# Kernel tuning notes

Measured on AMD Instinct MI355X. Metric: run time of the kernel, lower is better.

Reference implementation:

```python
import jax, jax.numpy as jnp
import numpy as np

NS = 150            # number of MC weight samples
D_IN, D_H, D_OUT = 1024, 512, 256


def setup_inputs() -> dict:
    key = jax.random.key(0)
    ks = jax.random.split(key, 9)
    x = jax.random.normal(ks[0], (32, D_IN), dtype=jnp.float32)
    # variational means (mu network params)
    mu_W1 = jax.random.normal(ks[1], (D_H, D_IN), dtype=jnp.float32) * 0.02
    mu_b1 = jnp.zeros((D_H,), dtype=jnp.float32)
    mu_W2 = jax.random.normal(ks[2], (D_OUT, D_H), dtype=jnp.float32) * 0.02
    mu_b2 = jnp.zeros((D_OUT,), dtype=jnp.float32)
    # variational log-stds (std network params v); std = exp(v)
    v_W1 = -3.0 + 0.1 * jax.random.normal(ks[3], (D_H, D_IN), dtype=jnp.float32)
    v_b1 = -3.0 + 0.1 * jax.random.normal(ks[4], (D_H,), dtype=jnp.float32)
    v_W2 = -3.0 + 0.1 * jax.random.normal(ks[5], (D_OUT, D_H), dtype=jnp.float32)
    v_b2 = -3.0 + 0.1 * jax.random.normal(ks[6], (D_OUT,), dtype=jnp.float32)
    return {
        "x": x,
        "mu_W1": mu_W1, "mu_b1": mu_b1, "mu_W2": mu_W2, "mu_b2": mu_b2,
        "v_W1": v_W1, "v_b1": v_b1, "v_W2": v_W2, "v_b2": v_b2,
    }


def reference(x, mu_W1, mu_b1, mu_W2, mu_b2, v_W1, v_b1, v_W2, v_b2):
    # Reparameterization: w = mu + eps * sqrt(exp(2v)) = mu + eps * exp(v)
    nk = jax.random.split(jax.random.key(42), 4)
    eW1 = jax.random.normal(nk[0], (NS,) + mu_W1.shape, dtype=mu_W1.dtype)
    eb1 = jax.random.normal(nk[1], (NS,) + mu_b1.shape, dtype=mu_b1.dtype)
    eW2 = jax.random.normal(nk[2], (NS,) + mu_W2.shape, dtype=mu_W2.dtype)
    eb2 = jax.random.normal(nk[3], (NS,) + mu_b2.shape, dtype=mu_b2.dtype)

    W1 = mu_W1 + eW1 * jnp.exp(v_W1)          # [ns, H, I]
    b1 = mu_b1 + eb1 * jnp.exp(v_b1)          # [ns, H]
    W2 = mu_W2 + eW2 * jnp.exp(v_W2)          # [ns, O, H]
    b2 = mu_b2 + eb2 * jnp.exp(v_b2)          # [ns, O]

    # MLP forward, batched over the ns sample axis
    h = jax.nn.relu(jnp.einsum('bi,nhi->nbh', x, W1) + b1[:, None, :])  # [ns, B, H]
    y = jnp.einsum('nbh,noh->nbo', h, W2) + b2[:, None, :]              # [ns, B, O]
    return y  # stacked MC outputs, [ns, B, O]
```

## Files before the change

kernel.cpp:

```cpp
#include <hip/hip_runtime.h>
#include <stdint.h>

#define NS 150
#define D_IN 1024
#define D_H 512
#define D_OUT 256

typedef __bf16 bf16x8 __attribute__((ext_vector_type(8)));
typedef float f32x4 __attribute__((ext_vector_type(4)));

#define OFF_XF    0u
#define OFF_MS1T  16384u
#define OFF_MS2T  1064960u
#define OFF_B1S   1327104u
#define OFF_B2S   1403904u
#define OFF_HB    1442304u

#define SQ2 1.41421354f

#define DSQ2 1.4142135623730951
#define DA  (-0.6931471805599453)
#define ZC3 ((float)(DSQ2 * -4.39150654e-06 * DA*DA*DA*DA*DA))
#define ZC4 ((float)(DSQ2 * 0.00021858087   * DA*DA*DA*DA))
#define ZC5 ((float)(DSQ2 * -0.00125372503  * DA*DA*DA))
#define ZC6 ((float)(DSQ2 * -0.00417768164  * DA*DA))
#define ZC7 ((float)(DSQ2 * 0.246640727     * DA))
#define ZC8 ((float)(DSQ2 * 1.50140941))
#define ZSHIFT 3.6067376022224085f
#define ZCUT  -7.213475204444817f

#define TT0 (SQ2 * -0.000200214257f)
#define TT1 (SQ2 * 0.000100950558f)
#define TT2 (SQ2 * 0.00134934322f)
#define TT3 (SQ2 * -0.00367342844f)
#define TT4 (SQ2 * 0.00573950773f)
#define TT5 (SQ2 * -0.0076224613f)
#define TT6 (SQ2 * 0.00943887047f)
#define TT7 (SQ2 * 1.00167406f)
#define TT8 (SQ2 * 2.83297682f)

#define ROTL32(x, r) __builtin_rotateleft32((x), (r))

__host__ __device__ __forceinline__ void threefry2x32(uint32_t k0, uint32_t k1,
                                                      uint32_t x0, uint32_t x1,
                                                      uint32_t& o0, uint32_t& o1) {
  uint32_t k2 = k0 ^ k1 ^ 0x1BD11BDAu;
  x0 += k0; x1 += k1;
#define TFR(r) { x0 += x1; x1 = ROTL32(x1, r); x1 ^= x0; }
  TFR(13) TFR(15) TFR(26) TFR(6)
  x0 += k1; x1 += k2 + 1u;
  TFR(17) TFR(29) TFR(16) TFR(24)
  x0 += k2; x1 += k0 + 2u;
  TFR(13) TFR(15) TFR(26) TFR(6)
  x0 += k0; x1 += k1 + 3u;
  TFR(17) TFR(29) TFR(16) TFR(24)
  x0 += k1; x1 += k2 + 4u;
  TFR(13) TFR(15) TFR(26) TFR(6)
  x0 += k2; x1 += k0 + 5u;
#undef TFR
  o0 = x0; o1 = x1;
}

__device__ __forceinline__ float tf_normal(uint32_t k0, uint32_t k1, uint32_t idx) {
  uint32_t o0, o1;
  threefry2x32(k0, k1, 0u, idx, o0, o1);
  uint32_t bits = o0 ^ o1;
  uint32_t fb = (bits >> 9) | 0x3F800000u;
  float m = __uint_as_float(fb);
  const float lo = -0.99999994f;
  float u = fmaxf(fmaf(m, 2.0f, -3.0f), lo);
  float t = fmaf(u, -u, 1.0f);
  float w = -0.69314718056f * __builtin_amdgcn_logf(t);
  float p;
  if (w < 5.0f) {
    float ww = w - 2.5f;
    p = SQ2 * 2.81022636e-08f;
    p = fmaf(p, ww, SQ2 * 3.43273939e-07f);
    p = fmaf(p, ww, SQ2 * -3.5233877e-06f);
    p = fmaf(p, ww, SQ2 * -4.39150654e-06f);
    p = fmaf(p, ww, SQ2 * 0.00021858087f);
    p = fmaf(p, ww, SQ2 * -0.00125372503f);
    p = fmaf(p, ww, SQ2 * -0.00417768164f);
    p = fmaf(p, ww, SQ2 * 0.246640727f);
    p = fmaf(p, ww, SQ2 * 1.50140941f);
  } else {
    float ww = __builtin_amdgcn_sqrtf(w) - 3.0f;
    p = TT0;
    p = fmaf(p, ww, TT1); p = fmaf(p, ww, TT2); p = fmaf(p, ww, TT3);
    p = fmaf(p, ww, TT4); p = fmaf(p, ww, TT5); p = fmaf(p, ww, TT6);
    p = fmaf(p, ww, TT7); p = fmaf(p, ww, TT8);
  }
  return p * u;
}

#define TF_ADD8 \
  "v_add_u32 %[a0], %[a0], %[b0]\n\t" "v_add_u32 %[a1], %[a1], %[b1]\n\t" \
  "v_add_u32 %[a2], %[a2], %[b2]\n\t" "v_add_u32 %[a3], %[a3], %[b3]\n\t" \
  "v_add_u32 %[a4], %[a4], %[b4]\n\t" "v_add_u32 %[a5], %[a5], %[b5]\n\t" \
  "v_add_u32 %[a6], %[a6], %[b6]\n\t" "v_add_u32 %[a7], %[a7], %[b7]\n\t"
#define TF_ROT8(sh) \
  "v_alignbit_b32 %[b0], %[b0], %[b0], " sh "\n\t" \
  "v_alignbit_b32 %[b1], %[b1], %[b1], " sh "\n\t" \
  "v_alignbit_b32 %[b2], %[b2], %[b2], " sh "\n\t" \
  "v_alignbit_b32 %[b3], %[b3], %[b3], " sh "\n\t" \
  "v_alignbit_b32 %[b4], %[b4], %[b4], " sh "\n\t" \
  "v_alignbit_b32 %[b5], %[b5], %[b5], " sh "\n\t" \
  "v_alignbit_b32 %[b6], %[b6], %[b6], " sh "\n\t" \
  "v_alignbit_b32 %[b7], %[b7], %[b7], " sh "\n\t"
#define TF_XOR8 \
  "v_xor_b32 %[b0], %[b0], %[a0]\n\t" "v_xor_b32 %[b1], %[b1], %[a1]\n\t" \
  "v_xor_b32 %[b2], %[b2], %[a2]\n\t" "v_xor_b32 %[b3], %[b3], %[a3]\n\t" \
  "v_xor_b32 %[b4], %[b4], %[a4]\n\t" "v_xor_b32 %[b5], %[b5], %[a5]\n\t" \
  "v_xor_b32 %[b6], %[b6], %[a6]\n\t" "v_xor_b32 %[b7], %[b7], %[a7]\n\t"
#define TF_ROUND(sh) TF_ADD8 TF_ROT8(sh) TF_XOR8
#define TF_R1(sh) \
  "v_add_u32 %[a0], %[k0], %[b0]\n\t" "v_add_u32 %[a1], %[k0], %[b1]\n\t" \
  "v_add_u32 %[a2], %[k0], %[b2]\n\t" "v_add_u32 %[a3], %[k0], %[b3]\n\t" \
  "v_add_u32 %[a4], %[k0], %[b4]\n\t" "v_add_u32 %[a5], %[k0], %[b5]\n\t" \
  "v_add_u32 %[a6], %[k0], %[b6]\n\t" "v_add_u32 %[a7], %[k0], %[b7]\n\t" \
  TF_ROT8(sh) TF_XOR8
#define TF_BADD8(KB) \
  "v_add_u32 %[b0], " KB ", %[b0]\n\t" "v_add_u32 %[b1], " KB ", %[b1]\n\t" \
  "v_add_u32 %[b2], " KB ", %[b2]\n\t" "v_add_u32 %[b3], " KB ", %[b3]\n\t" \
  "v_add_u32 %[b4], " KB ", %[b4]\n\t" "v_add_u32 %[b5], " KB ", %[b5]\n\t" \
  "v_add_u32 %[b6], " KB ", %[b6]\n\t" "v_add_u32 %[b7], " KB ", %[b7]\n\t"
#define TF_AADD8(KA) \
  "v_add_u32 %[a0], " KA ", %[a0]\n\t" "v_add_u32 %[a1], " KA ", %[a1]\n\t" \
  "v_add_u32 %[a2], " KA ", %[a2]\n\t" "v_add_u32 %[a3], " KA ", %[a3]\n\t" \
  "v_add_u32 %[a4], " KA ", %[a4]\n\t" "v_add_u32 %[a5], " KA ", %[a5]\n\t" \
  "v_add_u32 %[a6], " KA ", %[a6]\n\t" "v_add_u32 %[a7], " KA ", %[a7]\n\t"
#define TF_A3F(KA) \
  "v_add3_u32 %[a0], %[a0], %[b0], " KA "\n\t" \
  "v_add3_u32 %[a1], %[a1], %[b1], " KA "\n\t" \
  "v_add3_u32 %[a2], %[a2], %[b2], " KA "\n\t" \
  "v_add3_u32 %[a3], %[a3], %[b3], " KA "\n\t" \
  "v_add3_u32 %[a4], %[a4], %[b4], " KA "\n\t" \
  "v_add3_u32 %[a5], %[a5], %[b5], " KA "\n\t" \
  "v_add3_u32 %[a6], %[a6], %[b6], " KA "\n\t" \
  "v_add3_u32 %[a7], %[a7], %[b7], " KA "\n\t"
#define TF_RFOLD(KB, KA, sh) TF_BADD8(KB) TF_A3F(KA) TF_ROT8(sh) TF_XOR8

__device__ __forceinline__ void tf8_bits(uint32_t k0, uint32_t k1, uint32_t k2,
                                         uint32_t idx0, uint32_t* bits) {
  uint32_t k2p1 = k2 + 1u, k0p2 = k0 + 2u, k1p3 = k1 + 3u;
  uint32_t k2p4 = k2 + 4u, k0p5 = k0 + 5u;
  uint32_t t0 = idx0 + k1;
  uint32_t a0, a1, a2, a3, a4, a5, a6, a7;
  uint32_t b0 = t0, b1 = t0 + 1u, b2 = t0 + 2u, b3 = t0 + 3u;
  uint32_t b4 = t0 + 4u, b5 = t0 + 5u, b6 = t0 + 6u, b7 = t0 + 7u;
  asm(TF_R1("19") TF_ROUND("17") TF_ROUND("6") TF_ROUND("26")
      TF_RFOLD("%[k2p1]", "%[k1]", "15")
      TF_ROUND("3") TF_ROUND("16") TF_ROUND("8")
      TF_RFOLD("%[k0p2]", "%[k2]", "19")
      TF_ROUND("17") TF_ROUND("6") TF_ROUND("26")
      TF_RFOLD("%[k1p3]", "%[k0]", "15")
      TF_ROUND("3") TF_ROUND("16") TF_ROUND("8")
      TF_RFOLD("%[k2p4]", "%[k1]", "19")
      TF_ROUND("17") TF_ROUND("6") TF_ROUND("26")
      TF_AADD8("%[k2]") TF_BADD8("%[k0p5]")
      : [a0]"=&v"(a0), [a1]"=&v"(a1), [a2]"=&v"(a2), [a3]"=&v"(a3),
        [a4]"=&v"(a4), [a5]"=&v"(a5), [a6]"=&v"(a6), [a7]"=&v"(a7),
        [b0]"+v"(b0), [b1]"+v"(b1), [b2]"+v"(b2), [b3]"+v"(b3),
        [b4]"+v"(b4), [b5]"+v"(b5), [b6]"+v"(b6), [b7]"+v"(b7)
      : [k0]"s"(k0), [k1]"s"(k1), [k2]"s"(k2), [k2p1]"s"(k2p1),
        [k0p2]"s"(k0p2), [k1p3]"s"(k1p3), [k2p4]"s"(k2p4), [k0p5]"s"(k0p5));
  bits[0] = a0 ^ b0; bits[1] = a1 ^ b1; bits[2] = a2 ^ b2; bits[3] = a3 ^ b3;
  bits[4] = a4 ^ b4; bits[5] = a5 ^ b5; bits[6] = a6 ^ b6; bits[7] = a7 ^ b7;
}

__device__ __forceinline__ float bits_normal(uint32_t bits) {
  uint32_t fb = (bits >> 9) | 0x3F800000u;
  float m = __uint_as_float(fb);
  const float lo = -0.99999994f;
  float u = fmaxf(fmaf(m, 2.0f, -3.0f), lo);
  float t = fmaf(u, -u, 1.0f);
  float z = __builtin_amdgcn_logf(t);
  float p;
  if (z > ZCUT) {
    float zz = z + ZSHIFT;
    p = ZC3;
    p = fmaf(p, zz, ZC4); p = fmaf(p, zz, ZC5); p = fmaf(p, zz, ZC6);
    p = fmaf(p, zz, ZC7); p = fmaf(p, zz, ZC8);
  } else {
    float w = -0.69314718056f * z;
    float ww = __builtin_amdgcn_sqrtf(w) - 3.0f;
    p = TT0;
    p = fmaf(p, ww, TT1); p = fmaf(p, ww, TT2); p = fmaf(p, ww, TT3);
    p = fmaf(p, ww, TT4); p = fmaf(p, ww, TT5); p = fmaf(p, ww, TT6);
    p = fmaf(p, ww, TT7); p = fmaf(p, ww, TT8);
  }
  return p * u;
}

__global__ __launch_bounds__(256) void prep_kernel(
    const float* __restrict__ x,
    const float* __restrict__ muW1, const float* __restrict__ vW1,
    const float* __restrict__ muW2, const float* __restrict__ vW2,
    const float* __restrict__ mub1, const float* __restrict__ vb1,
    const float* __restrict__ mub2, const float* __restrict__ vb2,
    float* __restrict__ ws,
    uint32_t kb1_0, uint32_t kb1_1, uint32_t kb2_0, uint32_t kb2_1) {
  int bb = blockIdx.x;
  int tid = threadIdx.x;
  if (bb < 2048) {
    int t = bb * 256 + tid;
    ((float2*)(ws + OFF_MS1T))[t] = make_float2(muW1[t], expf(vW1[t]));
  } else if (bb < 2560) {
    int t = (bb - 2048) * 256 + tid;
    ((float2*)(ws + OFF_MS2T))[t] = make_float2(muW2[t], expf(vW2[t]));
  } else if (bb < 2688) {
    int t = (bb - 2560) * 256 + tid;
    int j = t & 7, lane = (t >> 3) & 63, fidx = t >> 9;
    int s = fidx >> 1, f = fidx & 1;
    int b = f * 16 + (lane & 15);
    int k = s * 32 + ((lane >> 4) << 3) + j;
    ((__bf16*)(ws + OFF_XF))[t] = (__bf16)x[b * D_IN + k];
  } else if (bb < 2988) {
    int t = (bb - 2688) * 256 + tid;
    int h = t & 511;
    float eps = tf_normal(kb1_0, kb1_1, (uint32_t)t);
    ws[OFF_B1S + t] = fmaf(eps, expf(vb1[h]), mub1[h]);
  } else {
    int t = (bb - 2988) * 256 + tid;
    int o = t & 255;
    float eps = tf_normal(kb2_0, kb2_1, (uint32_t)t);
    ws[OFF_B2S + t] = fmaf(eps, expf(vb2[o]), mub2[o]);
  }
}

__global__ __launch_bounds__(256) void l1_kernel(
    const float* __restrict__ ws, uint32_t k0, uint32_t k1) {
  const float2* __restrict__ ms1 = (const float2*)(ws + OFF_MS1T);
  const bf16x8* __restrict__ xf = (const bf16x8*)(ws + OFF_XF);
  const float* __restrict__ b1s = ws + OFF_B1S;
  __bf16* __restrict__ hB = (__bf16*)(ws + OFF_HB);
  uint32_t k2 = k0 ^ k1 ^ 0x1BD11BDAu;

  __shared__ f32x4 lred[2][2][64];

  int lane = threadIdx.x & 63;
  int wib = threadIdx.x >> 6;
  int pairIdx = wib >> 1, khalf = wib & 1;
  int tile = blockIdx.x * 2 + pairIdx;
  int n = tile >> 5;
  int ht = tile & 31;
  int mrow = lane & 15, quad = lane >> 4;
  int h = ht * 16 + mrow;
  uint32_t base = ((uint32_t)(n * 512 + h)) << 10;
  const float2* __restrict__ msrow = ms1 + (size_t)h * D_IN;

  f32x4 acc0 = {0.f, 0.f, 0.f, 0.f}, acc1 = {0.f, 0.f, 0.f, 0.f};

  int send = khalf * 16 + 16;
  for (int s = khalf * 16; s < send; ++s) {
    int kq = s * 32 + quad * 8;
    const f32x4* msq = (const f32x4*)(msrow + kq);
    f32x4 q0 = msq[0], q1 = msq[1], q2 = msq[2], q3 = msq[3];
    bf16x8 b0 = xf[(s * 2 + 0) * 64 + lane];
    bf16x8 b1 = xf[(s * 2 + 1) * 64 + lane];
    uint32_t bits[8];
    tf8_bits(k0, k1, k2, base + (uint32_t)kq, bits);
    float mu[8], sd[8];
    mu[0]=q0[0]; sd[0]=q0[1]; mu[1]=q0[2]; sd[1]=q0[3];
    mu[2]=q1[0]; sd[2]=q1[1]; mu[3]=q1[2]; sd[3]=q1[3];
    mu[4]=q2[0]; sd[4]=q2[1]; mu[5]=q2[2]; sd[5]=q2[3];
    mu[6]=q3[0]; sd[6]=q3[1]; mu[7]=q3[2]; sd[7]=q3[3];
    bf16x8 a;
#pragma unroll
    for (int j = 0; j < 8; ++j) {
      float eps = bits_normal(bits[j]);
      a[j] = (__bf16)fmaf(eps, sd[j], mu[j]);
    }
    acc0 = __builtin_amdgcn_mfma_f32_16x16x32_bf16(a, b0, acc0, 0, 0, 0);
    acc1 = __builtin_amdgcn_mfma_f32_16x16x32_bf16(a, b1, acc1, 0, 0, 0);
  }

  if (khalf) {
    lred[pairIdx][0][lane] = acc0;
    lred[pairIdx][1][lane] = acc1;
  }
  __syncthreads();
  if (!khalf) {
    f32x4 r0 = lred[pairIdx][0][lane], r1 = lred[pairIdx][1][lane];
    acc0 += r0; acc1 += r1;
    int hq = ht * 16 + quad * 4;
    float4 bias = *(const float4*)(b1s + n * 512 + hq);
    float bv[4] = {bias.x, bias.y, bias.z, bias.w};
    union { __bf16 v[4]; uint2 u; } p0, p1;
#pragma unroll
    for (int r = 0; r < 4; ++r) {
      p0.v[r] = (__bf16)fmaxf(acc0[r] + bv[r], 0.0f);
      p1.v[r] = (__bf16)fmaxf(acc1[r] + bv[r], 0.0f);
    }
    *(uint2*)(hB + ((size_t)(n * 32 + mrow) * 512 + hq)) = p0.u;
    *(uint2*)(hB + ((size_t)(n * 32 + 16 + mrow) * 512 + hq)) = p1.u;
  }
}

__global__ __launch_bounds__(256) void l2_kernel(
    const float* __restrict__ ws, float* __restrict__ y,
    uint32_t k0, uint32_t k1) {
  const float2* __restrict__ ms2 = (const float2*)(ws + OFF_MS2T);
  const bf16x8* __restrict__ hB8 = (const bf16x8*)(ws + OFF_HB);
  const float* __restrict__ b2s = ws + OFF_B2S;
  uint32_t k2 = k0 ^ k1 ^ 0x1BD11BDAu;

  __shared__ f32x4 lred[2][2][64];

  int lane = threadIdx.x & 63;
  int wib = threadIdx.x >> 6;
  int pairIdx = wib >> 1, khalf = wib & 1;
  int tile = blockIdx.x * 2 + pairIdx;
  int n = tile >> 4;
  int ot = tile & 15;
  int mrow = lane & 15, quad = lane >> 4;
  int o = ot * 16 + mrow;
  uint32_t base = (uint32_t)(n * 256 + o) << 9;
  const float2* __restrict__ msrow = ms2 + (size_t)o * D_H;

  f32x4 acc0 = {0.f, 0.f, 0.f, 0.f}, acc1 = {0.f, 0.f, 0.f, 0.f};

  int send = khalf * 8 + 8;
  for (int s = khalf * 8; s < send; ++s) {
    int kq = s * 32 + quad * 8;
    const f32x4* msq = (const f32x4*)(msrow + kq);
    f32x4 q0 = msq[0], q1 = msq[1], q2 = msq[2], q3 = msq[3];
    bf16x8 b0 = hB8[(size_t)(n * 32 + mrow) * 64 + s * 4 + quad];
    bf16x8 b1 = hB8[(size_t)(n * 32 + 16 + mrow) * 64 + s * 4 + quad];
    uint32_t bits[8];
    tf8_bits(k0, k1, k2, base + (uint32_t)kq, bits);
    float mu[8], sd[8];
    mu[0]=q0[0]; sd[0]=q0[1]; mu[1]=q0[2]; sd[1]=q0[3];
    mu[2]=q1[0]; sd[2]=q1[1]; mu[3]=q1[2]; sd[3]=q1[3];
    mu[4]=q2[0]; sd[4]=q2[1]; mu[5]=q2[2]; sd[5]=q2[3];
    mu[6]=q3[0]; sd[6]=q3[1]; mu[7]=q3[2]; sd[7]=q3[3];
    bf16x8 a;
#pragma unroll
    for (int j = 0; j < 8; ++j) {
      float eps = bits_normal(bits[j]);
      a[j] = (__bf16)fmaf(eps, sd[j], mu[j]);
    }
    acc0 = __builtin_amdgcn_mfma_f32_16x16x32_bf16(a, b0, acc0, 0, 0, 0);
    acc1 = __builtin_amdgcn_mfma_f32_16x16x32_bf16(a, b1, acc1, 0, 0, 0);
  }

  if (khalf) {
    lred[pairIdx][0][lane] = acc0;
    lred[pairIdx][1][lane] = acc1;
  }
  __syncthreads();
  if (!khalf) {
    f32x4 r0 = lred[pairIdx][0][lane], r1 = lred[pairIdx][1][lane];
    acc0 += r0; acc1 += r1;
    int oq = ot * 16 + quad * 4;
    float4 bias = *(const float4*)(b2s + n * 256 + oq);
    float4 o0, o1;
    o0.x = acc0[0] + bias.x; o0.y = acc0[1] + bias.y;
    o0.z = acc0[2] + bias.z; o0.w = acc0[3] + bias.w;
    o1.x = acc1[0] + bias.x; o1.y = acc1[1] + bias.y;
    o1.z = acc1[2] + bias.z; o1.w = acc1[3] + bias.w;
    *(float4*)(y + (size_t)(n * 32 + mrow) * 256 + oq) = o0;
    *(float4*)(y + (size_t)(n * 32 + 16 + mrow) * 256 + oq) = o1;
  }
}

extern "C" void kernel_launch(void* const* d_in, const int* in_sizes, int n_in,
                              void* d_out, int out_size, void* d_ws, size_t ws_size,
                              hipStream_t stream) {
  const float* x = (const float*)d_in[0];
  const float* muW1 = (const float*)d_in[1];
  const float* mub1 = (const float*)d_in[2];
  const float* muW2 = (const float*)d_in[3];
  const float* mub2 = (const float*)d_in[4];
  const float* vW1 = (const float*)d_in[5];
  const float* vb1 = (const float*)d_in[6];
  const float* vW2 = (const float*)d_in[7];
  const float* vb2 = (const float*)d_in[8];
  float* y = (float*)d_out;
  float* ws = (float*)d_ws;

  uint32_t nk[4][2];
  for (uint32_t j = 0; j < 4; ++j) {
    threefry2x32(0u, 42u, 0u, j, nk[j][0], nk[j][1]);
  }

  prep_kernel<<<3138, 256, 0, stream>>>(
      x, muW1, vW1, muW2, vW2, mub1, vb1, mub2, vb2, ws,
      nk[1][0], nk[1][1], nk[3][0], nk[3][1]);

  l1_kernel<<<2400, 256, 0, stream>>>(ws, nk[0][0], nk[0][1]);

  l2_kernel<<<1200, 256, 0, stream>>>(ws, y, nk[2][0], nk[2][1]);
}
```

Baseline: 296.5 us.

## Store hidden activations in MFMA fragment layout and use one tile per block

Layer 1 now writes the bf16 hidden activations straight into the fragment order that layer 2's MFMA B operand expects. Layer 2 can then read each fragment with one contiguous vector load per lane instead of gathering strided rows. Both kernels also shrink to 128-thread blocks that each handle a single tile, doubling the grid size. The layout change targets layer 2's load efficiency, and the smaller blocks let the two waves sync independently, at the cost of more blocks to schedule.

```diff
diff --git a/kernel.cpp b/kernel.cpp
--- a/kernel.cpp
+++ b/kernel.cpp
@@ -228,7 +228,7 @@
   }
 }
 
-__global__ __launch_bounds__(256) void l1_kernel(
+__global__ __launch_bounds__(128) void l1_kernel(
     const float* __restrict__ ws, uint32_t k0, uint32_t k1) {
   const float2* __restrict__ ms1 = (const float2*)(ws + OFF_MS1T);
   const bf16x8* __restrict__ xf = (const bf16x8*)(ws + OFF_XF);
@@ -236,12 +236,11 @@
   __bf16* __restrict__ hB = (__bf16*)(ws + OFF_HB);
   uint32_t k2 = k0 ^ k1 ^ 0x1BD11BDAu;
 
-  __shared__ f32x4 lred[2][2][64];
+  __shared__ f32x4 lred[2][64];
 
   int lane = threadIdx.x & 63;
-  int wib = threadIdx.x >> 6;
-  int pairIdx = wib >> 1, khalf = wib & 1;
-  int tile = blockIdx.x * 2 + pairIdx;
+  int khalf = threadIdx.x >> 6;
+  int tile = blockIdx.x;
   int n = tile >> 5;
   int ht = tile & 31;
   int mrow = lane & 15, quad = lane >> 4;
@@ -276,12 +275,12 @@
   }
 
   if (khalf) {
-    lred[pairIdx][0][lane] = acc0;
-    lred[pairIdx][1][lane] = acc1;
+    lred[0][lane] = acc0;
+    lred[1][lane] = acc1;
   }
   __syncthreads();
   if (!khalf) {
-    f32x4 r0 = lred[pairIdx][0][lane], r1 = lred[pairIdx][1][lane];
+    f32x4 r0 = lred[0][lane], r1 = lred[1][lane];
     acc0 += r0; acc1 += r1;
     int hq = ht * 16 + quad * 4;
     float4 bias = *(const float4*)(b1s + n * 512 + hq);
@@ -292,12 +291,14 @@
       p0.v[r] = (__bf16)fmaxf(acc0[r] + bv[r], 0.0f);
       p1.v[r] = (__bf16)fmaxf(acc1[r] + bv[r], 0.0f);
     }
-    *(uint2*)(hB + ((size_t)(n * 32 + mrow) * 512 + hq)) = p0.u;
-    *(uint2*)(hB + ((size_t)(n * 32 + 16 + mrow) * 512 + hq)) = p1.u;
-  }
-}
-
-__global__ __launch_bounds__(256) void l2_kernel(
+    size_t o0 = ((((size_t)(n * 16 + (ht >> 1)) * 2 + 0) * 4 +
+                  ((ht & 1) * 2 + (quad >> 1))) * 16 + mrow) * 8 + (quad & 1) * 4;
+    *(uint2*)(hB + o0) = p0.u;
+    *(uint2*)(hB + o0 + 512) = p1.u;
+  }
+}
+
+__global__ __launch_bounds__(128) void l2_kernel(
     const float* __restrict__ ws, float* __restrict__ y,
     uint32_t k0, uint32_t k1) {
   const float2* __restrict__ ms2 = (const float2*)(ws + OFF_MS2T);
@@ -305,12 +306,11 @@
   const float* __restrict__ b2s = ws + OFF_B2S;
   uint32_t k2 = k0 ^ k1 ^ 0x1BD11BDAu;
 
-  __shared__ f32x4 lred[2][2][64];
+  __shared__ f32x4 lred[2][64];
 
   int lane = threadIdx.x & 63;
-  int wib = threadIdx.x >> 6;
-  int pairIdx = wib >> 1, khalf = wib & 1;
-  int tile = blockIdx.x * 2 + pairIdx;
+  int khalf = threadIdx.x >> 6;
+  int tile = blockIdx.x;
   int n = tile >> 4;
   int ot = tile & 15;
   int mrow = lane & 15, quad = lane >> 4;
@@ -325,8 +325,9 @@
     int kq = s * 32 + quad * 8;
     const f32x4* msq = (const f32x4*)(msrow + kq);
     f32x4 q0 = msq[0], q1 = msq[1], q2 = msq[2], q3 = msq[3];
-    bf16x8 b0 = hB8[(size_t)(n * 32 + mrow) * 64 + s * 4 + quad];
-    bf16x8 b1 = hB8[(size_t)(n * 32 + 16 + mrow) * 64 + s * 4 + quad];
+    const bf16x8* hf = hB8 + (size_t)((n * 16 + s) * 2) * 64;
+    bf16x8 b0 = hf[lane];
+    bf16x8 b1 = hf[64 + lane];
     uint32_t bits[8];
     tf8_bits(k0, k1, k2, base + (uint32_t)kq, bits);
     float mu[8], sd[8];
@@ -345,12 +346,12 @@
   }
 
   if (khalf) {
-    lred[pairIdx][0][lane] = acc0;
-    lred[pairIdx][1][lane] = acc1;
+    lred[0][lane] = acc0;
+    lred[1][lane] = acc1;
   }
   __syncthreads();
   if (!khalf) {
-    f32x4 r0 = lred[pairIdx][0][lane], r1 = lred[pairIdx][1][lane];
+    f32x4 r0 = lred[0][lane], r1 = lred[1][lane];
     acc0 += r0; acc1 += r1;
     int oq = ot * 16 + quad * 4;
     float4 bias = *(const float4*)(b2s + n * 256 + oq);
@@ -388,7 +389,7 @@
       x, muW1, vW1, muW2, vW2, mub1, vb1, mub2, vb2, ws,
       nk[1][0], nk[1][1], nk[3][0], nk[3][1]);
 
-  l1_kernel<<<2400, 256, 0, stream>>>(ws, nk[0][0], nk[0][1]);
-
-  l2_kernel<<<1200, 256, 0, stream>>>(ws, y, nk[2][0], nk[2][1]);
-}
+  l1_kernel<<<4800, 128, 0, stream>>>(ws, nk[0][0], nk[0][1]);
+
+  l2_kernel<<<2400, 128, 0, stream>>>(ws, y, nk[2][0], nk[2][1]);
+}
```

Result: no change. 301.0 us (+1.5%).
